# Performance work log

Hardware: AMD Instinct MI355X
Metric: run time of the kernel (lower is better)

## Reference

```python
import jax, jax.numpy as jnp
import numpy as np

D_MODEL = 1024
N_HEADS = 16
D_K = D_MODEL // N_HEADS
B, T = 2, 2048


def setup_inputs() -> dict:
    key = jax.random.key(0)
    ks = jax.random.split(key, 12)
    s = 0.02
    return {
        "q": jax.random.normal(ks[0], (B, T, D_MODEL), jnp.float32),
        "k": jax.random.normal(ks[1], (B, T, D_MODEL), jnp.float32),
        "v": jax.random.normal(ks[2], (B, T, D_MODEL), jnp.float32),
        "Wq": jax.random.normal(ks[3], (D_MODEL, D_MODEL), jnp.float32) * s,
        "bq": jnp.zeros((D_MODEL,), jnp.float32),
        "Wk": jax.random.normal(ks[4], (D_MODEL, D_MODEL), jnp.float32) * s,
        "bk": jnp.zeros((D_MODEL,), jnp.float32),
        "Wv": jax.random.normal(ks[5], (D_MODEL, D_MODEL), jnp.float32) * s,
        "bv": jnp.zeros((D_MODEL,), jnp.float32),
        "Wo": jax.random.normal(ks[6], (D_MODEL, D_MODEL), jnp.float32) * s,
        "bo": jnp.zeros((D_MODEL,), jnp.float32),
        "mask": jnp.ones((B, T), jnp.int32),
        "causal": 1,
    }


def reference(q, k, v, Wq, bq, Wk, bk, Wv, bv, Wo, bo, mask, causal):
    Bq, Tq, D = q.shape
    Tk = k.shape[1]
    # projections (torch Linear: x @ W.T + b), split heads -> [B, H, T, d_k]
    qh = (q @ Wq.T + bq).reshape(Bq, Tq, N_HEADS, D_K).transpose(0, 2, 1, 3)
    kh = (k @ Wk.T + bk).reshape(Bq, Tk, N_HEADS, D_K).transpose(0, 2, 1, 3)
    vh = (v @ Wv.T + bv).reshape(Bq, Tk, N_HEADS, D_K).transpose(0, 2, 1, 3)
    scores = jnp.einsum("bhqd,bhkd->bhqk", qh, kh) / jnp.sqrt(jnp.float32(D_K))
    neg_inf = jnp.float32(-jnp.inf)
    if mask is not None:
        scores = jnp.where(mask[:, None, None, :] == 0, neg_inf, scores)
    if causal:
        causal_mask = jnp.tril(jnp.ones((Tq, Tq), jnp.float32))
        scores = jnp.where(causal_mask == 0, neg_inf, scores)
    attn = jax.nn.softmax(scores, axis=-1)
    out = jnp.einsum("bhqk,bhkd->bhqd", attn, vh)
    out = out.transpose(0, 2, 1, 3).reshape(Bq, Tq, D)
    return out @ Wo.T + bo
```

## Files before the change

### kernel.cpp

```cpp
#include <hip/hip_runtime.h>
#include <cstdint>
#include <cstddef>


typedef __bf16 bf16x8 __attribute__((ext_vector_type(8)));
typedef float f32x4 __attribute__((ext_vector_type(4)));

#define MFMA(a, b, c) __builtin_amdgcn_mfma_f32_16x16x32_bf16((a), (b), (c), 0, 0, 0)

static constexpr int D_MODEL = 1024;
static constexpr int T_ = 2048;
static constexpr int M_TOK = 4096;

__device__ __forceinline__ unsigned short f32_to_bf16(float f) {
    union { float f; uint32_t u; } v; v.f = f;
    uint32_t u = v.u;
    uint32_t r = u + 0x7fffu + ((u >> 16) & 1u);
    return (unsigned short)(r >> 16);
}
__device__ __forceinline__ unsigned f32_to_bf16_fast(float f) {
    union { float f; uint32_t u; } v; v.f = f;
    return (v.u + 0x8000u) >> 16;
}

typedef __attribute__((address_space(1))) void* as1_ptr;
typedef __attribute__((address_space(3))) void* as3_ptr;
__device__ __forceinline__ void gload_lds16(const void* g, void* l) {
    __builtin_amdgcn_global_load_lds((as1_ptr)(void*)g, (as3_ptr)l, 16, 0, 0);
}

__device__ __forceinline__ int keyperm(int k) {
    return (k & 32) | ((k & 12) << 1) | ((k & 16) >> 2) | (k & 3);
}

__global__ __launch_bounds__(256) void cvt_all(
    const float* __restrict__ q, const float* __restrict__ k,
    const float* __restrict__ v, const float* __restrict__ wq,
    const float* __restrict__ wk, const float* __restrict__ wv,
    const float* __restrict__ wo, ushort4* __restrict__ dst) {
    int i = blockIdx.x * blockDim.x + threadIdx.x;
    constexpr int R = 1 << 20;
    const float* s;
    int idx;
    if (i < 3 * R) {
        s = (i < R) ? q : (i < 2 * R) ? k : v;
        idx = i & (R - 1);
    } else {
        int j = i - 3 * R;
        int w = j >> 18;
        s = (w == 0) ? wq : (w == 1) ? wk : (w == 2) ? wv : wo;
        idx = j & ((1 << 18) - 1);
    }
    float4 f = ((const float4*)s)[idx];
    ushort4 o;
    o.x = (unsigned short)f32_to_bf16(f.x); o.y = (unsigned short)f32_to_bf16(f.y);
    o.z = (unsigned short)f32_to_bf16(f.z); o.w = (unsigned short)f32_to_bf16(f.w);
    dst[i] = o;
}

template<int MODE, int NT16>
__device__ __forceinline__ void gemm_body(
    const unsigned short* __restrict__ A, const unsigned short* __restrict__ W,
    const float* __restrict__ bias, void* __restrict__ outp,
    unsigned short* As, unsigned short* Ws, int bx, int by)
{
    constexpr bool SWAP = (MODE != 2);
    const int tid = threadIdx.x;
    const int lane = tid & 63, wave = tid >> 6;
    const int wm = wave >> 1, wn = wave & 1;
    const int r16 = lane & 15, kg = lane >> 4;
    const int m_blk = by * 128, n_blk = bx * (NT16 * 32);

    f32x4 acc[4][NT16];
    #pragma unroll
    for (int mt = 0; mt < 4; ++mt)
        #pragma unroll
        for (int nt = 0; nt < NT16; ++nt) acc[mt][nt] = (f32x4){0, 0, 0, 0};

    for (int k0 = 0; k0 < D_MODEL; k0 += 64) {
        __syncthreads();
        #pragma unroll
        for (int j = 0; j < 4; ++j) {
            int si = j * 256 + tid;
            int row = si >> 3, cg = (si & 7) ^ (row & 7);
            gload_lds16(A + (size_t)(m_blk + row) * D_MODEL + k0 + cg * 8,
                        (char*)As + (j * 256 + wave * 64) * 16);
        }
        #pragma unroll
        for (int j = 0; j < NT16; ++j) {
            int si = j * 256 + tid;
            int row = si >> 3, cg = (si & 7) ^ (row & 7);
            gload_lds16(W + (size_t)(n_blk + row) * D_MODEL + k0 + cg * 8,
                        (char*)Ws + (j * 256 + wave * 64) * 16);
        }
        __syncthreads();
        #pragma unroll
        for (int kc = 0; kc < 2; ++kc) {
            bf16x8 af[4], wf[NT16];
            #pragma unroll
            for (int mt = 0; mt < 4; ++mt) {
                int row = wm * 64 + mt * 16 + r16;
                af[mt] = *(const bf16x8*)(As + row * 64 + (((kc * 4 + kg) ^ (row & 7)) * 8));
            }
            #pragma unroll
            for (int nt = 0; nt < NT16; ++nt) {
                int row = wn * (NT16 * 16) + nt * 16 + r16;
                wf[nt] = *(const bf16x8*)(Ws + row * 64 + (((kc * 4 + kg) ^ (row & 7)) * 8));
            }
            #pragma unroll
            for (int mt = 0; mt < 4; ++mt)
                #pragma unroll
                for (int nt = 0; nt < NT16; ++nt)
                    acc[mt][nt] = SWAP ? MFMA(wf[nt], af[mt], acc[mt][nt])
                                       : MFMA(af[mt], wf[nt], acc[mt][nt]);
        }
    }
    if (MODE == 2) {
        #pragma unroll
        for (int nt = 0; nt < NT16; ++nt) {
            int n = n_blk + wn * (NT16 * 16) + nt * 16 + r16;
            float bn = bias[n];
            int hh = n >> 6, dki = n & 63;
            #pragma unroll
            for (int mt = 0; mt < 4; ++mt) {
                int m0 = m_blk + wm * 64 + mt * 16 + kg * 4;
                int mp = (m0 & ~63) | keyperm(m0 & 63);
                int bb = mp >> 11, ti = mp & 2047;
                ushort4 pk;
                pk.x = f32_to_bf16(acc[mt][nt][0] + bn);
                pk.y = f32_to_bf16(acc[mt][nt][1] + bn);
                pk.z = f32_to_bf16(acc[mt][nt][2] + bn);
                pk.w = f32_to_bf16(acc[mt][nt][3] + bn);
                *(ushort4*)((unsigned short*)outp +
                    ((size_t)(bb * 16 + hh) * 64 + dki) * 2048 + ti) = pk;
            }
        }
    } else {
        #pragma unroll
        for (int nt = 0; nt < NT16; ++nt) {
            int n0 = n_blk + wn * (NT16 * 16) + nt * 16 + kg * 4;
            float4 bn4 = *(const float4*)(bias + n0);
            #pragma unroll
            for (int mt = 0; mt < 4; ++mt) {
                int m = m_blk + wm * 64 + mt * 16 + r16;
                if (MODE == 3) {
                    float4 st;
                    st.x = acc[mt][nt][0] + bn4.x; st.y = acc[mt][nt][1] + bn4.y;
                    st.z = acc[mt][nt][2] + bn4.z; st.w = acc[mt][nt][3] + bn4.w;
                    *(float4*)((float*)outp + (size_t)m * D_MODEL + n0) = st;
                } else {
                    ushort4 pk;
                    pk.x = f32_to_bf16(acc[mt][nt][0] + bn4.x);
                    pk.y = f32_to_bf16(acc[mt][nt][1] + bn4.y);
                    pk.z = f32_to_bf16(acc[mt][nt][2] + bn4.z);
                    pk.w = f32_to_bf16(acc[mt][nt][3] + bn4.w);
                    *(ushort4*)((unsigned short*)outp + (size_t)m * D_MODEL + n0) = pk;
                }
            }
        }
    }
}

__global__ __launch_bounds__(256) void gemm_qkv(
    const unsigned short* __restrict__ qb, const unsigned short* __restrict__ kb,
    const unsigned short* __restrict__ vb, const unsigned short* __restrict__ Wqb,
    const unsigned short* __restrict__ Wkb, const unsigned short* __restrict__ Wvb,
    const float* __restrict__ bq, const float* __restrict__ bk, const float* __restrict__ bv,
    unsigned short* __restrict__ Qhp, unsigned short* __restrict__ Khp,
    unsigned short* __restrict__ Vtp)
{
    __shared__ __align__(16) unsigned short As[128 * 64];
    __shared__ __align__(16) unsigned short Ws[128 * 64];
    const int z = blockIdx.z;
    const unsigned short* A = (z == 0) ? qb : (z == 1) ? kb : vb;
    const unsigned short* W = (z == 0) ? Wqb : (z == 1) ? Wkb : Wvb;
    const float* bias = (z == 0) ? bq : (z == 1) ? bk : bv;
    if (z < 2)
        gemm_body<0, 4>(A, W, bias, (z == 0) ? (void*)Qhp : (void*)Khp, As, Ws,
                        blockIdx.x, blockIdx.y);
    else
        gemm_body<2, 4>(A, W, bias, (void*)Vtp, As, Ws, blockIdx.x, blockIdx.y);
}

__global__ __launch_bounds__(256) void gemm_out(
    const unsigned short* __restrict__ ab, const unsigned short* __restrict__ Wob,
    const float* __restrict__ bo, float* __restrict__ outp)
{
    __shared__ __align__(16) unsigned short As[128 * 64];
    __shared__ __align__(16) unsigned short Ws[64 * 64];
    gemm_body<3, 2>(ab, Wob, bo, (void*)outp, As, Ws, blockIdx.x, blockIdx.y);
}

__global__ __launch_bounds__(256) void attn_fwd(
    const unsigned short* __restrict__ Qh, const unsigned short* __restrict__ Kh,
    const unsigned short* __restrict__ Vt, const int* __restrict__ mask,
    const int* __restrict__ causal_p, unsigned short* __restrict__ attnout)
{
    __shared__ __align__(16) unsigned short Ks[2][64 * 64];
    __shared__ __align__(16) unsigned short Vs[2][64 * 64];

    const int tid = threadIdx.x;
    const int lane = tid & 63, wave = tid >> 6;
    const int bh = blockIdx.x;
    const int y = blockIdx.y, y0 = y & 7, j4 = y >> 3;
    const int qc = (j4 == 0) ? y0 : (j4 == 1) ? (15 - y0)
                 : (j4 == 2) ? (16 + y0) : (31 - y0);
    const int b = bh >> 4, h = bh & 15;
    const int causal = *causal_p;
    const int r16 = lane & 15, kg = lane >> 4;

    const int q0 = qc * 64 + wave * 16;

    const unsigned short* Qb = Qh + (size_t)b * T_ * D_MODEL + h * 64;
    const unsigned short* Kb = Kh + (size_t)b * T_ * D_MODEL + h * 64;
    const unsigned short* Vb = Vt + (size_t)bh * 64 * T_;
    const int* mb = mask + b * T_;

    bf16x8 qf0 = *(const bf16x8*)(Qb + (size_t)(q0 + r16) * D_MODEL + kg * 8);
    bf16x8 qf1 = *(const bf16x8*)(Qb + (size_t)(q0 + r16) * D_MODEL + 32 + kg * 8);

    float l = 0.f;
    f32x4 o[4];
    #pragma unroll
    for (int f = 0; f < 4; ++f) o[f] = (f32x4){0, 0, 0, 0};
    const float sc2 = 0.18033688011112042f;
    const int lim = wave * 16 + r16;

    const int nT = causal ? (qc + 1) : 32;

    auto stage = [&](int buf, int t) {
        int t0 = t * 64;
        #pragma unroll
        for (int j = 0; j < 2; ++j) {
            int si = j * 256 + tid;
            int row = si >> 3, cg = (si & 7) ^ (row & 7);
            gload_lds16(Kb + (size_t)(t0 + row) * D_MODEL + cg * 8,
                        (char*)Ks[buf] + (j * 256 + wave * 64) * 16);
            gload_lds16(Vb + (size_t)row * T_ + t0 + cg * 8,
                        (char*)Vs[buf] + (j * 256 + wave * 64) * 16);
        }
    };

    stage(0, 0);
    for (int t = 0; t < nT; ++t) {
        __syncthreads();
        if (t + 1 < nT) stage((t + 1) & 1, t + 1);
        const unsigned short* Kst = Ks[t & 1];
        const unsigned short* Vst = Vs[t & 1];
        const int t0 = t * 64;
        const bool diag = causal && (t == qc);

        unsigned long long km = __ballot(mb[t0 + lane] != 0);

        f32x4 s[4];
        #pragma unroll
        for (int c = 0; c < 4; ++c) {
            int key = c * 16 + r16;
            bf16x8 kf0 = *(const bf16x8*)(Kst + key * 64 + ((kg ^ (key & 7)) * 8));
            bf16x8 kf1 = *(const bf16x8*)(Kst + key * 64 + (((4 + kg) ^ (key & 7)) * 8));
            f32x4 z = (f32x4){0, 0, 0, 0};
            z = MFMA(kf0, qf0, z);
            z = MFMA(kf1, qf1, z);
            s[c] = z;
        }

        float pv[4][4];
        if (!diag && km == ~0ull) {
            #pragma unroll
            for (int c = 0; c < 4; ++c)
                #pragma unroll
                for (int r = 0; r < 4; ++r) {
                    float e = __builtin_amdgcn_exp2f(s[c][r] * sc2);
                    pv[c][r] = e; l += e;
                }
        } else {
            #pragma unroll
            for (int c = 0; c < 4; ++c) {
                unsigned mc = (unsigned)(km >> (c * 16));
                #pragma unroll
                for (int r = 0; r < 4; ++r) {
                    int kbit = kg * 4 + r;
                    bool ok = ((mc >> kbit) & 1) && (!diag || (c * 16 + kbit <= lim));
                    float e = ok ? __builtin_amdgcn_exp2f(s[c][r] * sc2) : 0.f;
                    pv[c][r] = e; l += e;
                }
            }
        }

        union pk_t { unsigned u[4]; bf16x8 v; };
        pk_t pa[2];
        #pragma unroll
        for (int c = 0; c < 4; ++c) {
            int half = (c & 1) * 2;
            pa[c >> 1].u[half]     = f32_to_bf16_fast(pv[c][0]) | (f32_to_bf16_fast(pv[c][1]) << 16);
            pa[c >> 1].u[half + 1] = f32_to_bf16_fast(pv[c][2]) | (f32_to_bf16_fast(pv[c][3]) << 16);
        }

        #pragma unroll
        for (int f = 0; f < 4; ++f) {
            int row = f * 16 + r16;
            int rx = row & 7;
            #pragma unroll
            for (int cp = 0; cp < 2; ++cp) {
                int g = cp * 4 + kg;
                bf16x8 vf = *(const bf16x8*)(Vst + row * 64 + ((g ^ rx) * 8));
                o[f] = MFMA(pa[cp].v, vf, o[f]);
            }
        }
    }

    l += __shfl_xor(l, 16, 64); l += __shfl_xor(l, 32, 64);
    float inv = (l > 0.f) ? 1.0f / l : 0.f;
    #pragma unroll
    for (int r = 0; r < 4; ++r) {
        int ql = kg * 4 + r;
        float iv = __shfl(inv, ql, 64);
        size_t base = ((size_t)(b * T_ + q0 + ql)) * D_MODEL + h * 64;
        #pragma unroll
        for (int f = 0; f < 4; ++f)
            attnout[base + f * 16 + r16] = f32_to_bf16(o[f][r] * iv);
    }
}

extern "C" void kernel_launch(void* const* d_in, const int* in_sizes, int n_in,
                              void* d_out, int out_size, void* d_ws, size_t ws_size,
                              hipStream_t stream) {
    const float* q  = (const float*)d_in[0];
    const float* k  = (const float*)d_in[1];
    const float* v  = (const float*)d_in[2];
    const float* Wq = (const float*)d_in[3];
    const float* bq = (const float*)d_in[4];
    const float* Wk = (const float*)d_in[5];
    const float* bk = (const float*)d_in[6];
    const float* Wv = (const float*)d_in[7];
    const float* bv = (const float*)d_in[8];
    const float* Wo = (const float*)d_in[9];
    const float* bo = (const float*)d_in[10];
    const int* mask   = (const int*)d_in[11];
    const int* causal = (const int*)d_in[12];

    const size_t SZ_TOK = (size_t)M_TOK * D_MODEL;
    const size_t SZ_W   = (size_t)D_MODEL * D_MODEL;

    unsigned short* qb  = (unsigned short*)d_ws;
    unsigned short* kb  = qb  + SZ_TOK;
    unsigned short* vb  = kb  + SZ_TOK;
    unsigned short* Wqb = vb  + SZ_TOK;
    unsigned short* Wkb = Wqb + SZ_W;
    unsigned short* Wvb = Wkb + SZ_W;
    unsigned short* Wob = Wvb + SZ_W;
    unsigned short* Qhp = Wob + SZ_W;
    unsigned short* Khp = Qhp + SZ_TOK;
    unsigned short* Vtp = Khp + SZ_TOK;
    unsigned short* ab  = Vtp + SZ_TOK;

    cvt_all<<<16384, 256, 0, stream>>>(q, k, v, Wq, Wk, Wv, Wo, (ushort4*)qb);

    gemm_qkv<<<dim3(D_MODEL / 128, M_TOK / 128, 3), 256, 0, stream>>>(
        qb, kb, vb, Wqb, Wkb, Wvb, bq, bk, bv, Qhp, Khp, Vtp);

    attn_fwd<<<dim3(32, 32), 256, 0, stream>>>(Qhp, Khp, Vtp, mask, causal, ab);

    gemm_out<<<dim3(D_MODEL / 64, M_TOK / 128), 256, 0, stream>>>(ab, Wob, bo,
                                                                  (float*)d_out);
}
```

Measured before the change: 225.1 us.

## Fuse fp32-to-bf16 activation conversion into QKV GEMM tile loads

```diff
diff --git a/kernel.cpp b/kernel.cpp
--- a/kernel.cpp
+++ b/kernel.cpp
@@ -18,9 +18,23 @@
     uint32_t r = u + 0x7fffu + ((u >> 16) & 1u);
     return (unsigned short)(r >> 16);
 }
-__device__ __forceinline__ unsigned f32_to_bf16_fast(float f) {
-    union { float f; uint32_t u; } v; v.f = f;
-    return (v.u + 0x8000u) >> 16;
+
+__device__ __forceinline__ unsigned pack2(float a, float b) {
+#if __has_builtin(__builtin_amdgcn_cvt_pk_bf16_f32)
+    typedef __bf16 bf16x2v __attribute__((ext_vector_type(2)));
+    union { bf16x2v v; unsigned u; } r;
+    r.v = __builtin_amdgcn_cvt_pk_bf16_f32(a, b);
+    return r.u;
+#else
+    union { float f; unsigned u; } x, y; x.f = a; y.f = b;
+    return ((x.u + 0x8000u) >> 16) | ((y.u + 0x8000u) & 0xffff0000u);
+#endif
+}
+__device__ __forceinline__ bf16x8 cvt8(f32x4 a, f32x4 b) {
+    union { unsigned u[4]; bf16x8 v; } r;
+    r.u[0] = pack2(a[0], a[1]); r.u[1] = pack2(a[2], a[3]);
+    r.u[2] = pack2(b[0], b[1]); r.u[3] = pack2(b[2], b[3]);
+    return r.v;
 }
 
 typedef __attribute__((address_space(1))) void* as1_ptr;
@@ -33,34 +47,23 @@
     return (k & 32) | ((k & 12) << 1) | ((k & 16) >> 2) | (k & 3);
 }
 
-__global__ __launch_bounds__(256) void cvt_all(
-    const float* __restrict__ q, const float* __restrict__ k,
-    const float* __restrict__ v, const float* __restrict__ wq,
-    const float* __restrict__ wk, const float* __restrict__ wv,
-    const float* __restrict__ wo, ushort4* __restrict__ dst) {
+__global__ __launch_bounds__(256) void cvt_w(
+    const float* __restrict__ wq, const float* __restrict__ wk,
+    const float* __restrict__ wv, const float* __restrict__ wo,
+    ushort4* __restrict__ dst) {
     int i = blockIdx.x * blockDim.x + threadIdx.x;
-    constexpr int R = 1 << 20;
-    const float* s;
-    int idx;
-    if (i < 3 * R) {
-        s = (i < R) ? q : (i < 2 * R) ? k : v;
-        idx = i & (R - 1);
-    } else {
-        int j = i - 3 * R;
-        int w = j >> 18;
-        s = (w == 0) ? wq : (w == 1) ? wk : (w == 2) ? wv : wo;
-        idx = j & ((1 << 18) - 1);
-    }
+    int w = i >> 18, idx = i & ((1 << 18) - 1);
+    const float* s = (w == 0) ? wq : (w == 1) ? wk : (w == 2) ? wv : wo;
     float4 f = ((const float4*)s)[idx];
     ushort4 o;
-    o.x = (unsigned short)f32_to_bf16(f.x); o.y = (unsigned short)f32_to_bf16(f.y);
-    o.z = (unsigned short)f32_to_bf16(f.z); o.w = (unsigned short)f32_to_bf16(f.w);
+    o.x = f32_to_bf16(f.x); o.y = f32_to_bf16(f.y);
+    o.z = f32_to_bf16(f.z); o.w = f32_to_bf16(f.w);
     dst[i] = o;
 }
 
-template<int MODE, int NT16>
+template<int MODE, int NT16, bool AFP32>
 __device__ __forceinline__ void gemm_body(
-    const unsigned short* __restrict__ A, const unsigned short* __restrict__ W,
+    const void* __restrict__ Ap, const unsigned short* __restrict__ W,
     const float* __restrict__ bias, void* __restrict__ outp,
     unsigned short* As, unsigned short* Ws, int bx, int by)
 {
@@ -71,6 +74,10 @@
     const int r16 = lane & 15, kg = lane >> 4;
     const int m_blk = by * 128, n_blk = bx * (NT16 * 32);
 
+    const float* Af = (const float*)Ap;
+    const unsigned short* Ab = (const unsigned short*)Ap;
+    float* Asf = (float*)As;
+
     f32x4 acc[4][NT16];
     #pragma unroll
     for (int mt = 0; mt < 4; ++mt)
@@ -79,12 +86,22 @@
 
     for (int k0 = 0; k0 < D_MODEL; k0 += 64) {
         __syncthreads();
-        #pragma unroll
-        for (int j = 0; j < 4; ++j) {
-            int si = j * 256 + tid;
-            int row = si >> 3, cg = (si & 7) ^ (row & 7);
-            gload_lds16(A + (size_t)(m_blk + row) * D_MODEL + k0 + cg * 8,
-                        (char*)As + (j * 256 + wave * 64) * 16);
+        if (AFP32) {
+            #pragma unroll
+            for (int j = 0; j < 8; ++j) {
+                int si = j * 256 + tid;
+                int row = si >> 4, ch = (si & 15) ^ (row & 15);
+                gload_lds16(Af + (size_t)(m_blk + row) * D_MODEL + k0 + ch * 4,
+                            (char*)As + (j * 256 + wave * 64) * 16);
+            }
+        } else {
+            #pragma unroll
+            for (int j = 0; j < 4; ++j) {
+                int si = j * 256 + tid;
+                int row = si >> 3, cg = (si & 7) ^ (row & 7);
+                gload_lds16(Ab + (size_t)(m_blk + row) * D_MODEL + k0 + cg * 8,
+                            (char*)As + (j * 256 + wave * 64) * 16);
+            }
         }
         #pragma unroll
         for (int j = 0; j < NT16; ++j) {
@@ -100,7 +117,14 @@
             #pragma unroll
             for (int mt = 0; mt < 4; ++mt) {
                 int row = wm * 64 + mt * 16 + r16;
-                af[mt] = *(const bf16x8*)(As + row * 64 + (((kc * 4 + kg) ^ (row & 7)) * 8));
+                if (AFP32) {
+                    int g = (kc * 4 + kg) * 2;
+                    f32x4 c0 = *(const f32x4*)(Asf + row * 64 + ((g ^ (row & 15)) * 4));
+                    f32x4 c1 = *(const f32x4*)(Asf + row * 64 + (((g + 1) ^ (row & 15)) * 4));
+                    af[mt] = cvt8(c0, c1);
+                } else {
+                    af[mt] = *(const bf16x8*)(As + row * 64 + (((kc * 4 + kg) ^ (row & 7)) * 8));
+                }
             }
             #pragma unroll
             for (int nt = 0; nt < NT16; ++nt) {
@@ -162,24 +186,25 @@
 }
 
 __global__ __launch_bounds__(256) void gemm_qkv(
-    const unsigned short* __restrict__ qb, const unsigned short* __restrict__ kb,
-    const unsigned short* __restrict__ vb, const unsigned short* __restrict__ Wqb,
+    const float* __restrict__ q, const float* __restrict__ k,
+    const float* __restrict__ v, const unsigned short* __restrict__ Wqb,
     const unsigned short* __restrict__ Wkb, const unsigned short* __restrict__ Wvb,
     const float* __restrict__ bq, const float* __restrict__ bk, const float* __restrict__ bv,
     unsigned short* __restrict__ Qhp, unsigned short* __restrict__ Khp,
     unsigned short* __restrict__ Vtp)
 {
-    __shared__ __align__(16) unsigned short As[128 * 64];
+    __shared__ __align__(16) unsigned short As[128 * 64 * 2];
     __shared__ __align__(16) unsigned short Ws[128 * 64];
     const int z = blockIdx.z;
-    const unsigned short* A = (z == 0) ? qb : (z == 1) ? kb : vb;
+    const float* A = (z == 0) ? q : (z == 1) ? k : v;
     const unsigned short* W = (z == 0) ? Wqb : (z == 1) ? Wkb : Wvb;
     const float* bias = (z == 0) ? bq : (z == 1) ? bk : bv;
     if (z < 2)
-        gemm_body<0, 4>(A, W, bias, (z == 0) ? (void*)Qhp : (void*)Khp, As, Ws,
-                        blockIdx.x, blockIdx.y);
+        gemm_body<0, 4, true>(A, W, bias, (z == 0) ? (void*)Qhp : (void*)Khp,
+                              As, Ws, blockIdx.x, blockIdx.y);
     else
-        gemm_body<2, 4>(A, W, bias, (void*)Vtp, As, Ws, blockIdx.x, blockIdx.y);
+        gemm_body<2, 4, true>(A, W, bias, (void*)Vtp, As, Ws,
+                              blockIdx.x, blockIdx.y);
 }
 
 __global__ __launch_bounds__(256) void gemm_out(
@@ -188,7 +213,8 @@
 {
     __shared__ __align__(16) unsigned short As[128 * 64];
     __shared__ __align__(16) unsigned short Ws[64 * 64];
-    gemm_body<3, 2>(ab, Wob, bo, (void*)outp, As, Ws, blockIdx.x, blockIdx.y);
+    gemm_body<3, 2, false>(ab, Wob, bo, (void*)outp, As, Ws,
+                           blockIdx.x, blockIdx.y);
 }
 
 __global__ __launch_bounds__(256) void attn_fwd(
@@ -292,8 +318,8 @@
         #pragma unroll
         for (int c = 0; c < 4; ++c) {
             int half = (c & 1) * 2;
-            pa[c >> 1].u[half]     = f32_to_bf16_fast(pv[c][0]) | (f32_to_bf16_fast(pv[c][1]) << 16);
-            pa[c >> 1].u[half + 1] = f32_to_bf16_fast(pv[c][2]) | (f32_to_bf16_fast(pv[c][3]) << 16);
+            pa[c >> 1].u[half]     = pack2(pv[c][0], pv[c][1]);
+            pa[c >> 1].u[half + 1] = pack2(pv[c][2], pv[c][3]);
         }
 
         #pragma unroll
@@ -342,10 +368,7 @@
     const size_t SZ_TOK = (size_t)M_TOK * D_MODEL;
     const size_t SZ_W   = (size_t)D_MODEL * D_MODEL;
 
-    unsigned short* qb  = (unsigned short*)d_ws;
-    unsigned short* kb  = qb  + SZ_TOK;
-    unsigned short* vb  = kb  + SZ_TOK;
-    unsigned short* Wqb = vb  + SZ_TOK;
+    unsigned short* Wqb = (unsigned short*)d_ws;
     unsigned short* Wkb = Wqb + SZ_W;
     unsigned short* Wvb = Wkb + SZ_W;
     unsigned short* Wob = Wvb + SZ_W;
@@ -354,10 +377,10 @@
     unsigned short* Vtp = Khp + SZ_TOK;
     unsigned short* ab  = Vtp + SZ_TOK;
 
-    cvt_all<<<16384, 256, 0, stream>>>(q, k, v, Wq, Wk, Wv, Wo, (ushort4*)qb);
+    cvt_w<<<4096, 256, 0, stream>>>(Wq, Wk, Wv, Wo, (ushort4*)Wqb);
 
     gemm_qkv<<<dim3(D_MODEL / 128, M_TOK / 128, 3), 256, 0, stream>>>(
-        qb, kb, vb, Wqb, Wkb, Wvb, bq, bk, bv, Qhp, Khp, Vtp);
+        q, k, v, Wqb, Wkb, Wvb, bq, bk, bv, Qhp, Khp, Vtp);
 
     attn_fwd<<<dim3(32, 32), 256, 0, stream>>>(Qhp, Khp, Vtp, mask, causal, ab);
 
```

Result: slower. 238.6 us (+6.0%).

## Double-buffer GEMM LDS tiles with BK=32 and use packed bf16 conversion in attention

Applied to the files above, without the earlier changes.

```diff
diff --git a/kernel.cpp b/kernel.cpp
--- a/kernel.cpp
+++ b/kernel.cpp
@@ -18,9 +18,17 @@
     uint32_t r = u + 0x7fffu + ((u >> 16) & 1u);
     return (unsigned short)(r >> 16);
 }
-__device__ __forceinline__ unsigned f32_to_bf16_fast(float f) {
-    union { float f; uint32_t u; } v; v.f = f;
-    return (v.u + 0x8000u) >> 16;
+
+__device__ __forceinline__ unsigned pack2(float a, float b) {
+#if __has_builtin(__builtin_amdgcn_cvt_pk_bf16_f32)
+    typedef __bf16 bf16x2v __attribute__((ext_vector_type(2)));
+    union { bf16x2v v; unsigned u; } r;
+    r.v = __builtin_amdgcn_cvt_pk_bf16_f32(a, b);
+    return r.u;
+#else
+    union { float f; unsigned u; } x, y; x.f = a; y.f = b;
+    return ((x.u + 0x8000u) >> 16) | ((y.u + 0x8000u) & 0xffff0000u);
+#endif
 }
 
 typedef __attribute__((address_space(1))) void* as1_ptr;
@@ -53,8 +61,8 @@
     }
     float4 f = ((const float4*)s)[idx];
     ushort4 o;
-    o.x = (unsigned short)f32_to_bf16(f.x); o.y = (unsigned short)f32_to_bf16(f.y);
-    o.z = (unsigned short)f32_to_bf16(f.z); o.w = (unsigned short)f32_to_bf16(f.w);
+    o.x = f32_to_bf16(f.x); o.y = f32_to_bf16(f.y);
+    o.z = f32_to_bf16(f.z); o.w = f32_to_bf16(f.w);
     dst[i] = o;
 }
 
@@ -65,6 +73,7 @@
     unsigned short* As, unsigned short* Ws, int bx, int by)
 {
     constexpr bool SWAP = (MODE != 2);
+    constexpr int NROW_W = NT16 * 32;
     const int tid = threadIdx.x;
     const int lane = tid & 63, wave = tid >> 6;
     const int wm = wave >> 1, wn = wave & 1;
@@ -77,44 +86,55 @@
         #pragma unroll
         for (int nt = 0; nt < NT16; ++nt) acc[mt][nt] = (f32x4){0, 0, 0, 0};
 
-    for (int k0 = 0; k0 < D_MODEL; k0 += 64) {
+    auto stage = [&](int buf, int ks) {
+        const int k0 = ks * 32;
+        unsigned short* Ab = As + buf * (128 * 32);
+        unsigned short* Wb = Ws + buf * (NROW_W * 32);
+        #pragma unroll
+        for (int j = 0; j < 2; ++j) {
+            int si = j * 256 + tid;
+            int row = si >> 2;
+            int ch = (si & 3) ^ (row & 3) ^ ((row >> 2) & 3);
+            gload_lds16(A + (size_t)(m_blk + row) * D_MODEL + k0 + ch * 8,
+                        (char*)Ab + (j * 256 + wave * 64) * 16);
+        }
+        #pragma unroll
+        for (int j = 0; j < NROW_W / 64; ++j) {
+            int si = j * 256 + tid;
+            int row = si >> 2;
+            int ch = (si & 3) ^ (row & 3) ^ ((row >> 2) & 3);
+            gload_lds16(W + (size_t)(n_blk + row) * D_MODEL + k0 + ch * 8,
+                        (char*)Wb + (j * 256 + wave * 64) * 16);
+        }
+    };
+
+    stage(0, 0);
+    for (int ks = 0; ks < 32; ++ks) {
         __syncthreads();
-        #pragma unroll
-        for (int j = 0; j < 4; ++j) {
-            int si = j * 256 + tid;
-            int row = si >> 3, cg = (si & 7) ^ (row & 7);
-            gload_lds16(A + (size_t)(m_blk + row) * D_MODEL + k0 + cg * 8,
-                        (char*)As + (j * 256 + wave * 64) * 16);
-        }
-        #pragma unroll
-        for (int j = 0; j < NT16; ++j) {
-            int si = j * 256 + tid;
-            int row = si >> 3, cg = (si & 7) ^ (row & 7);
-            gload_lds16(W + (size_t)(n_blk + row) * D_MODEL + k0 + cg * 8,
-                        (char*)Ws + (j * 256 + wave * 64) * 16);
-        }
-        __syncthreads();
-        #pragma unroll
-        for (int kc = 0; kc < 2; ++kc) {
-            bf16x8 af[4], wf[NT16];
-            #pragma unroll
-            for (int mt = 0; mt < 4; ++mt) {
-                int row = wm * 64 + mt * 16 + r16;
-                af[mt] = *(const bf16x8*)(As + row * 64 + (((kc * 4 + kg) ^ (row & 7)) * 8));
-            }
-            #pragma unroll
-            for (int nt = 0; nt < NT16; ++nt) {
-                int row = wn * (NT16 * 16) + nt * 16 + r16;
-                wf[nt] = *(const bf16x8*)(Ws + row * 64 + (((kc * 4 + kg) ^ (row & 7)) * 8));
-            }
-            #pragma unroll
-            for (int mt = 0; mt < 4; ++mt)
-                #pragma unroll
-                for (int nt = 0; nt < NT16; ++nt)
-                    acc[mt][nt] = SWAP ? MFMA(wf[nt], af[mt], acc[mt][nt])
-                                       : MFMA(af[mt], wf[nt], acc[mt][nt]);
-        }
-    }
+        if (ks + 1 < 32) stage((ks + 1) & 1, ks + 1);
+        const unsigned short* Ab = As + (ks & 1) * (128 * 32);
+        const unsigned short* Wb = Ws + (ks & 1) * (NROW_W * 32);
+        bf16x8 af[4], wf[NT16];
+        #pragma unroll
+        for (int mt = 0; mt < 4; ++mt) {
+            int row = wm * 64 + mt * 16 + r16;
+            int fx = (row & 3) ^ ((row >> 2) & 3);
+            af[mt] = *(const bf16x8*)(Ab + row * 32 + ((kg ^ fx) * 8));
+        }
+        #pragma unroll
+        for (int nt = 0; nt < NT16; ++nt) {
+            int row = wn * (NT16 * 16) + nt * 16 + r16;
+            int fx = (row & 3) ^ ((row >> 2) & 3);
+            wf[nt] = *(const bf16x8*)(Wb + row * 32 + ((kg ^ fx) * 8));
+        }
+        #pragma unroll
+        for (int mt = 0; mt < 4; ++mt)
+            #pragma unroll
+            for (int nt = 0; nt < NT16; ++nt)
+                acc[mt][nt] = SWAP ? MFMA(wf[nt], af[mt], acc[mt][nt])
+                                   : MFMA(af[mt], wf[nt], acc[mt][nt]);
+    }
+
     if (MODE == 2) {
         #pragma unroll
         for (int nt = 0; nt < NT16; ++nt) {
@@ -169,15 +189,15 @@
     unsigned short* __restrict__ Qhp, unsigned short* __restrict__ Khp,
     unsigned short* __restrict__ Vtp)
 {
-    __shared__ __align__(16) unsigned short As[128 * 64];
-    __shared__ __align__(16) unsigned short Ws[128 * 64];
+    __shared__ __align__(16) unsigned short As[2 * 128 * 32];
+    __shared__ __align__(16) unsigned short Ws[2 * 128 * 32];
     const int z = blockIdx.z;
     const unsigned short* A = (z == 0) ? qb : (z == 1) ? kb : vb;
     const unsigned short* W = (z == 0) ? Wqb : (z == 1) ? Wkb : Wvb;
     const float* bias = (z == 0) ? bq : (z == 1) ? bk : bv;
     if (z < 2)
-        gemm_body<0, 4>(A, W, bias, (z == 0) ? (void*)Qhp : (void*)Khp, As, Ws,
-                        blockIdx.x, blockIdx.y);
+        gemm_body<0, 4>(A, W, bias, (z == 0) ? (void*)Qhp : (void*)Khp,
+                        As, Ws, blockIdx.x, blockIdx.y);
     else
         gemm_body<2, 4>(A, W, bias, (void*)Vtp, As, Ws, blockIdx.x, blockIdx.y);
 }
@@ -186,8 +206,8 @@
     const unsigned short* __restrict__ ab, const unsigned short* __restrict__ Wob,
     const float* __restrict__ bo, float* __restrict__ outp)
 {
-    __shared__ __align__(16) unsigned short As[128 * 64];
-    __shared__ __align__(16) unsigned short Ws[64 * 64];
+    __shared__ __align__(16) unsigned short As[2 * 128 * 32];
+    __shared__ __align__(16) unsigned short Ws[2 * 64 * 32];
     gemm_body<3, 2>(ab, Wob, bo, (void*)outp, As, Ws, blockIdx.x, blockIdx.y);
 }
 
@@ -292,8 +312,8 @@
         #pragma unroll
         for (int c = 0; c < 4; ++c) {
             int half = (c & 1) * 2;
-            pa[c >> 1].u[half]     = f32_to_bf16_fast(pv[c][0]) | (f32_to_bf16_fast(pv[c][1]) << 16);
-            pa[c >> 1].u[half + 1] = f32_to_bf16_fast(pv[c][2]) | (f32_to_bf16_fast(pv[c][3]) << 16);
+            pa[c >> 1].u[half]     = pack2(pv[c][0], pv[c][1]);
+            pa[c >> 1].u[half + 1] = pack2(pv[c][2], pv[c][3]);
         }
 
         #pragma unroll
```

New measurement: 229.8 us. 2.1% more time.
